# Kernel tuning notes

Hardware: AMD Instinct MI355X
Metric: run time of the kernel (lower is better)

The kernel has to match this reference:

```python
import jax, jax.numpy as jnp
import numpy as np

B, T, C = 512, 80, 512      # batch, encoder seq len, in_channels
H = 256                     # hidden_size
V = 6625                    # out_channels / num_classes


def setup_inputs() -> dict:
    key = jax.random.key(0)
    ks = jax.random.split(key, 12)
    s = lambda *shape: 1.0 / np.sqrt(shape[-1])
    inputs = jax.random.normal(ks[0], (B, T, C), dtype=jnp.float32)
    targets = jax.random.randint(ks[1], (B, 25), 0, V, dtype=jnp.int64)
    i2h_w = jax.random.normal(ks[2], (H, C), dtype=jnp.float32) * s(H, C)
    h2h_w = jax.random.normal(ks[3], (H, H), dtype=jnp.float32) * s(H, H)
    h2h_b = jax.random.normal(ks[4], (H,), dtype=jnp.float32) * 0.01
    score_w = jax.random.normal(ks[5], (1, H), dtype=jnp.float32) * s(1, H)
    gru_in = C + V
    gru_wih = jax.random.normal(ks[6], (3 * H, gru_in), dtype=jnp.float32) * s(3 * H, gru_in)
    gru_whh = jax.random.normal(ks[7], (3 * H, H), dtype=jnp.float32) * s(3 * H, H)
    gru_bih = jax.random.normal(ks[8], (3 * H,), dtype=jnp.float32) * 0.01
    gru_bhh = jax.random.normal(ks[9], (3 * H,), dtype=jnp.float32) * 0.01
    gen_w = jax.random.normal(ks[10], (V, H), dtype=jnp.float32) * s(V, H)
    gen_b = jax.random.normal(ks[11], (V,), dtype=jnp.float32) * 0.01
    return {"inputs": inputs, "targets": targets, "batch_max_length": 25,
            "i2h_w": i2h_w, "h2h_w": h2h_w, "h2h_b": h2h_b, "score_w": score_w,
            "gru_wih": gru_wih, "gru_whh": gru_whh, "gru_bih": gru_bih,
            "gru_bhh": gru_bhh, "gen_w": gen_w, "gen_b": gen_b}


def reference(inputs, targets, batch_max_length, i2h_w, h2h_w, h2h_b, score_w,
              gru_wih, gru_whh, gru_bih, gru_bhh, gen_w, gen_b):
    # batch_H projection is step-invariant: same math as per-step i2h(batch_H)
    batch_H_proj = jnp.einsum('btc,hc->bth', inputs, i2h_w)  # [B,T,H]
    hidden0 = jnp.zeros((inputs.shape[0], H), dtype=inputs.dtype)

    def step(hidden, tgt_t):
        # Bahdanau attention
        ph = hidden @ h2h_w.T + h2h_b                          # [B,H]
        res = jnp.tanh(batch_H_proj + ph[:, None, :])          # [B,T,H]
        e = jnp.einsum('bth,oh->bt', res, score_w)             # [B,T] (score has out dim 1)
        alpha = jax.nn.softmax(e, axis=1)                      # softmax over T
        context = jnp.einsum('bt,btc->bc', alpha, inputs)      # [B,C]
        onehot = jax.nn.one_hot(tgt_t, V, dtype=inputs.dtype)  # [B,V]
        x = jnp.concatenate([context, onehot], axis=1)         # [B,C+V]
        # PyTorch GRUCell
        gi = x @ gru_wih.T + gru_bih                           # [B,3H]
        gh = hidden @ gru_whh.T + gru_bhh                      # [B,3H]
        i_r, i_z, i_n = jnp.split(gi, 3, axis=1)
        h_r, h_z, h_n = jnp.split(gh, 3, axis=1)
        r = jax.nn.sigmoid(i_r + h_r)
        z = jax.nn.sigmoid(i_z + h_z)
        n = jnp.tanh(i_n + r * h_n)
        new_h = (1.0 - z) * n + z * hidden
        return new_h, new_h

    num_steps = batch_max_length
    _, hiddens = jax.lax.scan(step, hidden0, targets[:, :num_steps].T)  # [S,B,H]
    output = jnp.transpose(hiddens, (1, 0, 2))                          # [B,S,H]
    probs = jnp.einsum('bsh,vh->bsv', output, gen_w) + gen_b            # [B,S,V]
    return probs
```

## Files before the change

kernel.cpp:

```cpp
#include <hip/hip_runtime.h>
#include <hip/hip_bf16.h>
#include <hip/hip_fp16.h>
#include <cstdint>

constexpr int kB = 512;
constexpr int kT = 80;
constexpr int kC = 512;
constexpr int kH = 256;
constexpr int kV = 6625;
constexpr int kGIN = kC + kV;

typedef __attribute__((ext_vector_type(8))) short short8;
typedef __attribute__((ext_vector_type(4))) float floatx4;
typedef _Float16 h2v __attribute__((ext_vector_type(2)));
typedef _Float16 half8 __attribute__((ext_vector_type(8)));

__device__ __forceinline__ float fast_tanh(float x) {
  float e = __expf(2.f * x);
  return 1.f - 2.f / (e + 1.f);
}
__device__ __forceinline__ float fast_sig(float x) {
  return 1.f / (1.f + __expf(-x));
}
__device__ __forceinline__ float2 h2f(unsigned int u) {
  union { unsigned int u; __half2 h; } cvt; cvt.u = u;
  return __half22float2(cvt.h);
}
__device__ __forceinline__ h2v as_h2v(unsigned int u) {
  union { unsigned int u; h2v h; } c; c.u = u; return c.h;
}
__device__ __forceinline__ float fdot2f(unsigned int a, unsigned int b, float c) {
#if __has_builtin(__builtin_amdgcn_fdot2)
  return __builtin_amdgcn_fdot2(as_h2v(a), as_h2v(b), c, false);
#else
  h2v av = as_h2v(a), bv = as_h2v(b);
  return (float)av[0] * (float)bv[0] + (float)av[1] * (float)bv[1] + c;
#endif
}

__device__ __forceinline__ void gld_lds16(const void* g, void* l) {
  __builtin_amdgcn_global_load_lds(
      (const __attribute__((address_space(1))) void*)(uintptr_t)g,
      (__attribute__((address_space(3))) void*)(uintptr_t)l, 16, 0, 0);
}

__global__ __launch_bounds__(256) void cvt_bf16(const float* __restrict__ x,
                                                __hip_bfloat16* __restrict__ y,
                                                int n) {
  int i = blockIdx.x * 256 + threadIdx.x;
  if (i < n) y[i] = __float2bfloat16(x[i]);
}

__global__ __launch_bounds__(256) void cvt_fp16x4(const float* __restrict__ x,
                                                  __half* __restrict__ y) {
  int i = (blockIdx.x * 256 + threadIdx.x) * 4;
  float4 v = *(const float4*)(x + i);
  __half2 h01 = __floats2half2_rn(v.x, v.y);
  __half2 h23 = __floats2half2_rn(v.z, v.w);
  uint2 u;
  u.x = *reinterpret_cast<unsigned int*>(&h01);
  u.y = *reinterpret_cast<unsigned int*>(&h23);
  *(uint2*)(y + i) = u;
}

__global__ __launch_bounds__(256) void cvt_wh(const float* __restrict__ h2h,
                                              const float* __restrict__ whh,
                                              __half* __restrict__ wH) {
  const int n = blockIdx.x, c = threadIdx.x;
  float v = (n < kH) ? h2h[(size_t)n * kH + c] : whh[(size_t)(n - kH) * kH + c];
  wH[(size_t)n * kH + c] = __float2half(v);
}

__global__ __launch_bounds__(256) void cvt_wih(const float* __restrict__ wih,
                                               __half* __restrict__ wihH) {
  const int n = blockIdx.x, t = threadIdx.x;
  wihH[(size_t)n * kC + t] = __float2half(wih[(size_t)n * kGIN + t]);
  wihH[(size_t)n * kC + 256 + t] = __float2half(wih[(size_t)n * kGIN + 256 + t]);
}

__global__ __launch_bounds__(256) void wt_transpose(const float* __restrict__ wih,
                                                    const float* __restrict__ bih,
                                                    float* __restrict__ WT) {
  __shared__ float tile[32][33];
  const int vb = blockIdx.x * 32, nb = blockIdx.y * 32;
  const int tx = threadIdx.x & 31, ty0 = threadIdx.x >> 5;
#pragma unroll
  for (int i = 0; i < 4; ++i) {
    int n = nb + ty0 + i * 8;
    int v = vb + tx;
    tile[ty0 + i * 8][tx] = (v < kV) ? wih[(size_t)n * kGIN + kC + v] : 0.f;
  }
  __syncthreads();
  const float bb = bih[nb + tx];
#pragma unroll
  for (int i = 0; i < 4; ++i) {
    int v = vb + ty0 + i * 8;
    if (v < kV) WT[(size_t)v * 768 + nb + tx] = tile[tx][ty0 + i * 8] + bb;
  }
}

__global__ __launch_bounds__(256) void proj_gemm_f16(
    const __half* __restrict__ A, const __half* __restrict__ W,
    __half* __restrict__ C) {
  constexpr int K = kC, ldc = kH;
  __shared__ __align__(16) _Float16 As[128 * 32];
  __shared__ __align__(16) _Float16 Ws[128 * 32];
  const int tid = threadIdx.x;
  const int wave = tid >> 6, lane = tid & 63;
  const int m0 = blockIdx.x * 128, n0 = blockIdx.y * 128;
  floatx4 acc[4][4] = {};
  const int lr = lane & 15;
  const int lkb = (lane >> 4) * 8;
  const int mloc = (wave & 1) * 64;
  const int nloc = (wave >> 1) * 64;
  const int srow = wave * 16 + (lane >> 2);
  const int skq = (lane & 3) * 8;
  for (int kt = 0; kt < K; kt += 32) {
#pragma unroll
    for (int r = 0; r < 2; ++r) {
      int rowA = r * 64 + srow;
      const __half* ga = A + (size_t)(m0 + rowA) * K + kt + skq;
      gld_lds16(ga, (char*)As + (size_t)(r * 64 + wave * 16) * 64);
      const __half* gw = W + (size_t)(n0 + rowA) * K + kt + skq;
      gld_lds16(gw, (char*)Ws + (size_t)(r * 64 + wave * 16) * 64);
    }
    __syncthreads();
    half8 af[4], wf[4];
#pragma unroll
    for (int i = 0; i < 4; ++i)
      af[i] = *(const half8*)(As + (mloc + i * 16 + lr) * 32 + lkb);
#pragma unroll
    for (int j = 0; j < 4; ++j)
      wf[j] = *(const half8*)(Ws + (nloc + j * 16 + lr) * 32 + lkb);
#pragma unroll
    for (int i = 0; i < 4; ++i)
#pragma unroll
      for (int j = 0; j < 4; ++j)
        acc[i][j] = __builtin_amdgcn_mfma_f32_16x16x32_f16(af[i], wf[j], acc[i][j], 0, 0, 0);
    __syncthreads();
  }
#pragma unroll
  for (int i = 0; i < 4; ++i) {
#pragma unroll
    for (int j = 0; j < 4; ++j) {
      int col = n0 + nloc + j * 16 + lr;
      int rowb = m0 + mloc + i * 16 + ((lane >> 4) << 2);
#pragma unroll
      for (int r = 0; r < 4; ++r)
        C[(size_t)(rowb + r) * ldc + col] = __float2half(acc[i][j][r]);
    }
  }
}

__global__ __launch_bounds__(512, 2) void fused_steps(
    const __half* __restrict__ inH,
    const __half* __restrict__ projH,
    const int*   __restrict__ targets,
    const __half* __restrict__ wHp,
    const float* __restrict__ h2h_b, const float* __restrict__ bhh,
    const __half* __restrict__ wihHp,
    const float* __restrict__ WT,
    const float* __restrict__ score_w,
    __hip_bfloat16* __restrict__ hidd,
    int S) {
  __shared__ __align__(16) float hid_s[kH];
  __shared__ __align__(16) _Float16 hidh_s[kH];
  __shared__ __align__(16) float phgh_s[1024];
  __shared__ __align__(16) _Float16 ctxh_s[kC];
  __shared__ __align__(16) float cst[kC];
  __shared__ __align__(16) float gi_s[768];
  __shared__ float e_s[kT];
  const int tid = threadIdx.x;
  const int bid = blockIdx.x;
  const int r0 = bid;
  const int wave = tid >> 6, lane = tid & 63;
  const int g = tid >> 3, q = tid & 7;
  const _Float16* wH = (const _Float16*)wHp;
  const _Float16* wihH = (const _Float16*)wihHp;

  if (tid < kH) { hid_s[tid] = 0.f; hidh_s[tid] = (_Float16)0.f; }

  const float4 s4 = *(const float4*)(score_w + lane * 4);

  uint2 pr[10];
#pragma unroll
  for (int k = 0; k < 10; ++k) {
    const int t = wave + 8 * k;
    pr[k] = *(const uint2*)(projH + ((size_t)r0 * kT + t) * kH + lane * 4);
  }
  __syncthreads();

  const int rot = bid % 12;

  for (int s = 0; s < S; ++s) {
#pragma unroll
    for (int i = 0; i < 4; ++i) {
      const int n = g + (((i + bid) & 3) << 6);
      const _Float16* wr = wH + (size_t)n * kH;
      float a0 = 0.f;
#pragma unroll
      for (int p = 0; p < 4; ++p) {
        const int c = p * 64 + q * 8;
        uint4 wv = *(const uint4*)(wr + c);
        uint4 hv = *(const uint4*)(&hidh_s[c]);
        a0 = fdot2f(wv.x, hv.x, a0);
        a0 = fdot2f(wv.y, hv.y, a0);
        a0 = fdot2f(wv.z, hv.z, a0);
        a0 = fdot2f(wv.w, hv.w, a0);
      }
      a0 += __shfl_xor(a0, 1); a0 += __shfl_xor(a0, 2); a0 += __shfl_xor(a0, 4);
      if (q == 0) phgh_s[n] = a0 + h2h_b[n];
    }
    __syncthreads();

    {
      float4 ph4 = *(const float4*)(&phgh_s[lane * 4]);
#pragma unroll
      for (int k = 0; k < 10; ++k) {
        const int t = wave + 8 * k;
        float2 p01 = h2f(pr[k].x), p23 = h2f(pr[k].y);
        float part = fast_tanh(p01.x + ph4.x) * s4.x +
                     fast_tanh(p01.y + ph4.y) * s4.y +
                     fast_tanh(p23.x + ph4.z) * s4.z +
                     fast_tanh(p23.y + ph4.w) * s4.w;
#pragma unroll
        for (int off = 32; off > 0; off >>= 1) part += __shfl_xor(part, off);
        if (lane == 0) e_s[t] = part;
      }
    }
    __syncthreads();

    if (wave == 0) {
      float v0 = e_s[lane];
      float v1 = (lane < kT - 64) ? e_s[64 + lane] : -1e30f;
      float mx = fmaxf(v0, v1);
#pragma unroll
      for (int off = 32; off > 0; off >>= 1) mx = fmaxf(mx, __shfl_xor(mx, off));
      float x0 = __expf(v0 - mx);
      float x1 = (lane < kT - 64) ? __expf(v1 - mx) : 0.f;
      float sm = x0 + x1;
#pragma unroll
      for (int off = 32; off > 0; off >>= 1) sm += __shfl_xor(sm, off);
      float inv = 1.f / sm;
      e_s[lane] = x0 * inv;
      if (lane < kT - 64) e_s[64 + lane] = x1 * inv;
    }
    __syncthreads();

    {
      const int sub = tid >> 8, c2 = (tid & 255) * 2;
      const __half* ib = inH + (size_t)r0 * kT * kC + c2;
      float a0 = 0.f, a1 = 0.f;
      const int t0 = sub * 40;
#pragma unroll 4
      for (int t = t0; t < t0 + 40; ++t) {
        const float al = e_s[t];
        float2 v = h2f(*(const unsigned int*)(ib + (size_t)t * kC));
        a0 += al * v.x; a1 += al * v.y;
      }
      if (sub) { cst[c2] = a0; cst[c2 + 1] = a1; }
      __syncthreads();
      if (!sub) {
        ctxh_s[c2] = (_Float16)(a0 + cst[c2]);
        ctxh_s[c2 + 1] = (_Float16)(a1 + cst[c2 + 1]);
      }
    }
    __syncthreads();

#pragma unroll 2
    for (int i = 0; i < 12; ++i) {
      int io = i + rot; if (io >= 12) io -= 12;
      const int n = g + (io << 6);
      const _Float16* wr = wihH + (size_t)n * kC;
      float a0 = 0.f, b0 = 0.f;
#pragma unroll
      for (int p = 0; p < 8; p += 2) {
        const int c0 = p * 64 + q * 8;
        const int c1 = c0 + 64;
        uint4 wv0 = *(const uint4*)(wr + c0);
        uint4 wv1 = *(const uint4*)(wr + c1);
        uint4 xv0 = *(const uint4*)(&ctxh_s[c0]);
        uint4 xv1 = *(const uint4*)(&ctxh_s[c1]);
        a0 = fdot2f(wv0.x, xv0.x, a0);
        a0 = fdot2f(wv0.y, xv0.y, a0);
        a0 = fdot2f(wv0.z, xv0.z, a0);
        a0 = fdot2f(wv0.w, xv0.w, a0);
        b0 = fdot2f(wv1.x, xv1.x, b0);
        b0 = fdot2f(wv1.y, xv1.y, b0);
        b0 = fdot2f(wv1.z, xv1.z, b0);
        b0 = fdot2f(wv1.w, xv1.w, b0);
      }
      a0 += b0;
      a0 += __shfl_xor(a0, 1); a0 += __shfl_xor(a0, 2); a0 += __shfl_xor(a0, 4);
      if (q == 0) gi_s[n] = a0;
    }
#pragma unroll 2
    for (int i = 0; i < 12; ++i) {
      int io = i + rot; if (io >= 12) io -= 12;
      const int m = g + (io << 6);
      const _Float16* wr = wH + (size_t)(256 + m) * kH;
      float a0 = 0.f;
#pragma unroll
      for (int p = 0; p < 4; ++p) {
        const int c = p * 64 + q * 8;
        uint4 wv = *(const uint4*)(wr + c);
        uint4 hv = *(const uint4*)(&hidh_s[c]);
        a0 = fdot2f(wv.x, hv.x, a0);
        a0 = fdot2f(wv.y, hv.y, a0);
        a0 = fdot2f(wv.z, hv.z, a0);
        a0 = fdot2f(wv.w, hv.w, a0);
      }
      a0 += __shfl_xor(a0, 1); a0 += __shfl_xor(a0, 2); a0 += __shfl_xor(a0, 4);
      if (q == 0) phgh_s[256 + m] = a0 + bhh[m];
    }
    __syncthreads();

    if (tid < kH) {
      const int h = tid;
      const int tg = targets[(size_t)r0 * S + s];
      const float* wtr = WT + (size_t)tg * 768;
      float i_r = gi_s[h] + wtr[h];
      float i_z = gi_s[kH + h] + wtr[kH + h];
      float i_n = gi_s[2 * kH + h] + wtr[2 * kH + h];
      float h_r = phgh_s[kH + h];
      float h_z = phgh_s[2 * kH + h];
      float h_n = phgh_s[3 * kH + h];
      float hv = hid_s[h];
      float rr = fast_sig(i_r + h_r);
      float z = fast_sig(i_z + h_z);
      float nn = fast_tanh(i_n + rr * h_n);
      float o = (1.f - z) * nn + z * hv;
      hid_s[h] = o;
      hidh_s[h] = (_Float16)o;
      hidd[((size_t)r0 * S + s) * kH + h] = __float2bfloat16(o);
    }
    __syncthreads();
  }
}

__global__ __launch_bounds__(256) void final_gemm(
    const __hip_bfloat16* __restrict__ A, const __hip_bfloat16* __restrict__ W,
    const float* __restrict__ bias, float* __restrict__ C, int M, int N, int K) {
  __shared__ __align__(16) short As[128 * 32];
  __shared__ __align__(16) short Ws[128 * 32];
  const int tid = threadIdx.x;
  const int wave = tid >> 6, lane = tid & 63;
  const int u = blockIdx.x;
  const int idx = (u & 7) * 650 + (u >> 3);
  const int m0 = (idx % 100) * 128, n0 = (idx / 100) * 128;
  floatx4 acc[4][4] = {};
  const int lr = lane & 15;
  const int lkb = (lane >> 4) * 8;
  const int mloc = (wave & 1) * 64;
  const int nloc = (wave >> 1) * 64;
  const int srow = wave * 16 + (lane >> 2);
  const int skq = (lane & 3) * 8;
  for (int kt = 0; kt < K; kt += 32) {
#pragma unroll
    for (int r = 0; r < 2; ++r) {
      int rowA = r * 64 + srow;
      const __hip_bfloat16* ga = A + (size_t)(m0 + rowA) * K + kt + skq;
      gld_lds16(ga, (char*)As + (size_t)(r * 64 + wave * 16) * 64);
      int rowW = n0 + rowA;
      if (rowW > N - 1) rowW = N - 1;
      const __hip_bfloat16* gw = W + (size_t)rowW * K + kt + skq;
      gld_lds16(gw, (char*)Ws + (size_t)(r * 64 + wave * 16) * 64);
    }
    __syncthreads();
    short8 af[4], wf[4];
#pragma unroll
    for (int i = 0; i < 4; ++i)
      af[i] = *(const short8*)(As + (mloc + i * 16 + lr) * 32 + lkb);
#pragma unroll
    for (int j = 0; j < 4; ++j)
      wf[j] = *(const short8*)(Ws + (nloc + j * 16 + lr) * 32 + lkb);
#pragma unroll
    for (int i = 0; i < 4; ++i)
#pragma unroll
      for (int j = 0; j < 4; ++j)
        acc[i][j] = __builtin_amdgcn_mfma_f32_16x16x32_bf16(af[i], wf[j], acc[i][j], 0, 0, 0);
    __syncthreads();
  }
#pragma unroll
  for (int i = 0; i < 4; ++i) {
#pragma unroll
    for (int j = 0; j < 4; ++j) {
      int col = n0 + nloc + j * 16 + lr;
      if (col < N) {
        int rowb = m0 + mloc + i * 16 + ((lane >> 4) << 2);
        float bs = bias[col];
#pragma unroll
        for (int r = 0; r < 4; ++r)
          C[(size_t)(rowb + r) * N + col] = acc[i][j][r] + bs;
      }
    }
  }
}

extern "C" void kernel_launch(void* const* d_in, const int* in_sizes, int n_in,
                              void* d_out, int out_size, void* d_ws, size_t ws_size,
                              hipStream_t stream) {
  const float* inputs  = (const float*)d_in[0];
  const int*   targets = (const int*)d_in[1];
  const float* i2h_w   = (const float*)d_in[3];
  const float* h2h_w   = (const float*)d_in[4];
  const float* h2h_b   = (const float*)d_in[5];
  const float* score_w = (const float*)d_in[6];
  const float* gru_wih = (const float*)d_in[7];
  const float* gru_whh = (const float*)d_in[8];
  const float* gru_bih = (const float*)d_in[9];
  const float* gru_bhh = (const float*)d_in[10];
  const float* gen_w   = (const float*)d_in[11];
  const float* gen_b   = (const float*)d_in[12];
  float* out = (float*)d_out;
  const int S = out_size / (kB * kV);

  char* ws = (char*)d_ws;
  size_t off = 0;
  auto alloc = [&](size_t bytes) {
    void* p = ws + off;
    off += (bytes + 255) & ~(size_t)255;
    return p;
  };
  __half* projH = (__half*)alloc((size_t)kB * kT * kH * 2);
  float* WT   = (float*)alloc((size_t)kV * 768 * 4);
  __half* inH = (__half*)alloc((size_t)kB * kT * kC * 2);
  __half* wH  = (__half*)alloc((size_t)1024 * kH * 2);
  __half* wihH = (__half*)alloc((size_t)768 * kC * 2);
  __half* i2hH = (__half*)alloc((size_t)kH * kC * 2);
  __hip_bfloat16* hidd = (__hip_bfloat16*)alloc((size_t)kB * S * kH * 2);
  __hip_bfloat16* gw16 = (__hip_bfloat16*)alloc((size_t)kV * kH * 2);

  cvt_bf16<<<dim3((kV * kH + 255) / 256), 256, 0, stream>>>(gen_w, gw16, kV * kH);
  cvt_fp16x4<<<dim3(kB * kT * kC / 4 / 256), 256, 0, stream>>>(inputs, inH);
  cvt_fp16x4<<<dim3(kH * kC / 4 / 256), 256, 0, stream>>>(i2h_w, i2hH);
  cvt_wh<<<dim3(1024), 256, 0, stream>>>(h2h_w, gru_whh, wH);
  cvt_wih<<<dim3(768), 256, 0, stream>>>(gru_wih, wihH);
  wt_transpose<<<dim3((kV + 31) / 32, 768 / 32), 256, 0, stream>>>(gru_wih, gru_bih, WT);

  proj_gemm_f16<<<dim3(kB * kT / 128, kH / 128), 256, 0, stream>>>(inH, i2hH, projH);

  fused_steps<<<dim3(kB), 512, 0, stream>>>(
      inH, projH, targets, wH, h2h_b, gru_bhh, wihH, WT, score_w, hidd, S);

  final_gemm<<<dim3(100 * 52), 256, 0, stream>>>(
      hidd, gw16, gen_b, out, kB * S, kV, kH);
}
```

Measured before the change: 1.553 ms.

## Warp-specialize step loop: overlap hidden-GRU matvec with attention phases

Splits the 8 waves per block so waves 0-3 handle the attention score, softmax and context over all 80 timesteps, while waves 4-7 compute the hidden-to-hidden GRU matvec in three chunks alongside those phases. This replaces a separate serial gh loop after the gi matvec and drops the two-half context reduction along with its shared buffer. The goal is to hide the latency-bound attention phases behind independent matvec work. In exchange, the attention work runs on half as many waves and each of those threads keeps 20 projection registers instead of 10, which raises register pressure.

Result: slower. 3.298 ms (+112.4%).

```diff
diff --git a/kernel.cpp b/kernel.cpp
--- a/kernel.cpp
+++ b/kernel.cpp
@@ -152,6 +152,29 @@
   }
 }
 
+#define GH_CHUNK(cidx)                                                        \
+  {                                                                           \
+    const int g2 = (tid >> 3) - 32;                                           \
+    for (int j = 0; j < 8; ++j) {                                             \
+      int jj = (cidx) * 8 + j + rot24; if (jj >= 24) jj -= 24;                \
+      const int m = g2 + (jj << 5);                                           \
+      const _Float16* wr = wH + (size_t)(256 + m) * kH;                       \
+      float a0 = 0.f;                                                         \
+      _Pragma("unroll")                                                       \
+      for (int p = 0; p < 4; ++p) {                                           \
+        const int c = p * 64 + q * 8;                                         \
+        uint4 wv = *(const uint4*)(wr + c);                                   \
+        uint4 hv = *(const uint4*)(&hidh_s[c]);                               \
+        a0 = fdot2f(wv.x, hv.x, a0);                                          \
+        a0 = fdot2f(wv.y, hv.y, a0);                                          \
+        a0 = fdot2f(wv.z, hv.z, a0);                                          \
+        a0 = fdot2f(wv.w, hv.w, a0);                                          \
+      }                                                                       \
+      a0 += __shfl_xor(a0, 1); a0 += __shfl_xor(a0, 2); a0 += __shfl_xor(a0, 4); \
+      if (q == 0) phgh_s[256 + m] = a0 + bhh[m];                              \
+    }                                                                         \
+  }
+
 __global__ __launch_bounds__(512, 2) void fused_steps(
     const __half* __restrict__ inH,
     const __half* __restrict__ projH,
@@ -167,7 +190,6 @@
   __shared__ __align__(16) _Float16 hidh_s[kH];
   __shared__ __align__(16) float phgh_s[1024];
   __shared__ __align__(16) _Float16 ctxh_s[kC];
-  __shared__ __align__(16) float cst[kC];
   __shared__ __align__(16) float gi_s[768];
   __shared__ float e_s[kT];
   const int tid = threadIdx.x;
@@ -182,15 +204,18 @@
 
   const float4 s4 = *(const float4*)(score_w + lane * 4);
 
-  uint2 pr[10];
-#pragma unroll
-  for (int k = 0; k < 10; ++k) {
-    const int t = wave + 8 * k;
-    pr[k] = *(const uint2*)(projH + ((size_t)r0 * kT + t) * kH + lane * 4);
+  uint2 pr[20];
+  if (wave < 4) {
+#pragma unroll
+    for (int k = 0; k < 20; ++k) {
+      const int t = wave + 4 * k;
+      pr[k] = *(const uint2*)(projH + ((size_t)r0 * kT + t) * kH + lane * 4);
+    }
   }
   __syncthreads();
 
   const int rot = bid % 12;
+  const int rot24 = bid % 24;
 
   for (int s = 0; s < S; ++s) {
 #pragma unroll
@@ -213,11 +238,11 @@
     }
     __syncthreads();
 
-    {
+    if (wave < 4) {
       float4 ph4 = *(const float4*)(&phgh_s[lane * 4]);
 #pragma unroll
-      for (int k = 0; k < 10; ++k) {
-        const int t = wave + 8 * k;
+      for (int k = 0; k < 20; ++k) {
+        const int t = wave + 4 * k;
         float2 p01 = h2f(pr[k].x), p23 = h2f(pr[k].y);
         float part = fast_tanh(p01.x + ph4.x) * s4.x +
                      fast_tanh(p01.y + ph4.y) * s4.y +
@@ -227,7 +252,7 @@
         for (int off = 32; off > 0; off >>= 1) part += __shfl_xor(part, off);
         if (lane == 0) e_s[t] = part;
       }
-    }
+    } else GH_CHUNK(0)
     __syncthreads();
 
     if (wave == 0) {
@@ -244,27 +269,22 @@
       float inv = 1.f / sm;
       e_s[lane] = x0 * inv;
       if (lane < kT - 64) e_s[64 + lane] = x1 * inv;
-    }
-    __syncthreads();
-
-    {
-      const int sub = tid >> 8, c2 = (tid & 255) * 2;
+    } else if (wave >= 4) GH_CHUNK(1)
+    __syncthreads();
+
+    if (wave < 4) {
+      const int c2 = tid * 2;
       const __half* ib = inH + (size_t)r0 * kT * kC + c2;
       float a0 = 0.f, a1 = 0.f;
-      const int t0 = sub * 40;
 #pragma unroll 4
-      for (int t = t0; t < t0 + 40; ++t) {
+      for (int t = 0; t < kT; ++t) {
         const float al = e_s[t];
         float2 v = h2f(*(const unsigned int*)(ib + (size_t)t * kC));
         a0 += al * v.x; a1 += al * v.y;
       }
-      if (sub) { cst[c2] = a0; cst[c2 + 1] = a1; }
-      __syncthreads();
-      if (!sub) {
-        ctxh_s[c2] = (_Float16)(a0 + cst[c2]);
-        ctxh_s[c2 + 1] = (_Float16)(a1 + cst[c2 + 1]);
-      }
-    }
+      ctxh_s[c2] = (_Float16)a0;
+      ctxh_s[c2 + 1] = (_Float16)a1;
+    } else GH_CHUNK(2)
     __syncthreads();
 
 #pragma unroll 2
@@ -294,25 +314,6 @@
       a0 += __shfl_xor(a0, 1); a0 += __shfl_xor(a0, 2); a0 += __shfl_xor(a0, 4);
       if (q == 0) gi_s[n] = a0;
     }
-#pragma unroll 2
-    for (int i = 0; i < 12; ++i) {
-      int io = i + rot; if (io >= 12) io -= 12;
-      const int m = g + (io << 6);
-      const _Float16* wr = wH + (size_t)(256 + m) * kH;
-      float a0 = 0.f;
-#pragma unroll
-      for (int p = 0; p < 4; ++p) {
-        const int c = p * 64 + q * 8;
-        uint4 wv = *(const uint4*)(wr + c);
-        uint4 hv = *(const uint4*)(&hidh_s[c]);
-        a0 = fdot2f(wv.x, hv.x, a0);
-        a0 = fdot2f(wv.y, hv.y, a0);
-        a0 = fdot2f(wv.z, hv.z, a0);
-        a0 = fdot2f(wv.w, hv.w, a0);
-      }
-      a0 += __shfl_xor(a0, 1); a0 += __shfl_xor(a0, 2); a0 += __shfl_xor(a0, 4);
-      if (q == 0) phgh_s[256 + m] = a0 + bhh[m];
-    }
     __syncthreads();
 
     if (tid < kH) {
```
